# Kernel optimization log

Hardware: AMD Instinct MI355X
Metric: run time of the kernel (lower is better)

Reference implementation:

```python
import jax, jax.numpy as jnp
import numpy as np

B, I, O, S, C = 64, 2048, 2048, 10, 512  # batch, input, output, dendritic segments, context dim


def setup_inputs() -> dict:
    key = jax.random.key(0)
    ks = jax.random.split(key, 8)
    x = jax.random.normal(ks[0], (B, I), dtype=jnp.float32)
    context = jax.random.normal(ks[1], (B, C), dtype=jnp.float32)
    prev_activation = jax.random.normal(ks[2], (B, I), dtype=jnp.float32)
    # sparse-initialized weight: randn/sqrt(I) * (rand > sparsity)
    w = jax.random.normal(ks[3], (O, I), dtype=jnp.float32) / np.sqrt(I)
    mask = (jax.random.uniform(ks[4], (O, I)) > 0.9).astype(jnp.float32)
    weight = w * mask
    bias = jnp.zeros((O,), dtype=jnp.float32)
    astrocyte_activation = jnp.ones((O,), dtype=jnp.float32)
    astrocyte_threshold = jnp.full((O,), 0.5, dtype=jnp.float32)
    dendrite_segments = jax.random.normal(ks[5], (O, I, S), dtype=jnp.float32) / np.sqrt(I)
    dendritic_gates = jnp.ones((O, S), dtype=jnp.float32)
    connection_strength = jnp.ones((O, I), dtype=jnp.float32)
    pruning_threshold = jnp.full((1,), 0.01, dtype=jnp.float32)
    return {
        "x": x, "context": context, "prev_activation": prev_activation,
        "weight": weight, "bias": bias,
        "astrocyte_activation": astrocyte_activation,
        "astrocyte_threshold": astrocyte_threshold,
        "dendrite_segments": dendrite_segments,
        "dendritic_gates": dendritic_gates,
        "connection_strength": connection_strength,
        "pruning_threshold": pruning_threshold,
    }


def reference(x, context, prev_activation, weight, bias, astrocyte_activation,
              astrocyte_threshold, dendrite_segments, dendritic_gates,
              connection_strength, pruning_threshold):
    dt = x.dtype
    # structural plasticity (eval branch): prune weak connections
    conn_mask = (jnp.abs(weight) * connection_strength > pruning_threshold[0]).astype(dt)
    eff_w = weight * conn_mask  # [O, I]
    # astrocyte modulation
    ctx_signal = jnp.mean(context, axis=-1, keepdims=True)          # [B, 1]
    astro = jax.nn.sigmoid(ctx_signal * astrocyte_activation[None, :])  # [B, O]
    astro = astro * (astro > astrocyte_threshold[None, :]).astype(dt)
    mean_astro = jnp.mean(astro, axis=0)                            # [O]
    mod_w = eff_w * mean_astro[:, None]                             # [O, I]
    synaptic = x @ mod_w.T + bias                                   # [B, O]
    # multi-compartment dendritic processing
    seg_act = jnp.einsum('bi,ois->bos', x, dendrite_segments)       # [B, O, S]
    gated = jax.nn.relu(seg_act) * jax.nn.sigmoid(dendritic_gates)[None, :, :]
    dendritic = jnp.sum(gated, axis=-1)                             # [B, O]
    return jax.nn.relu(synaptic + dendritic)
```

## Files before the change

kernel.cpp:

```cpp
#include <hip/hip_runtime.h>
#include <math.h>

#define Bn 64
#define In 2048
#define On 2048
#define Sn 10
#define Cn 512

#define OT 4
#define KSPLIT 4
#define KRANGE (In / KSPLIT)
#define KT 64
#define NSTG (KRANGE / KT)
#define LROW 72
#define SLOT 12

typedef short short8 __attribute__((ext_vector_type(8)));
typedef float f32x4 __attribute__((ext_vector_type(4)));

__device__ __forceinline__ unsigned short f2bf(float f) {
    union { float f; unsigned u; } v; v.f = f;
    unsigned r = (v.u + 0x7FFFu + ((v.u >> 16) & 1u)) >> 16;
    return (unsigned short)r;
}

__global__ void prep_kernel(const float* __restrict__ x,
                            const float* __restrict__ ctx,
                            float* __restrict__ ws_ctx,
                            unsigned short* __restrict__ ws_xbf) {
    const int b = blockIdx.x;
    const int t = threadIdx.x;
    if (b < Bn) {
        __shared__ float red[256];
        red[t] = ctx[b * Cn + t] + ctx[b * Cn + t + 256];
        __syncthreads();
        for (int off = 128; off > 0; off >>= 1) {
            if (t < off) red[t] += red[t + off];
            __syncthreads();
        }
        if (t == 0) ws_ctx[b] = red[0] * (1.0f / (float)Cn);
    } else {
        int idx = (b - Bn) * 256 + t;
        ws_xbf[idx] = f2bf(x[idx]);
    }
}

__global__ void mastro_kernel(const float* __restrict__ aact,
                              const float* __restrict__ athr,
                              const float* __restrict__ ws_ctx,
                              float* __restrict__ ws_mastro) {
    const int o = blockIdx.x * 256 + threadIdx.x;
    const float aa = aact[o], th = athr[o];
    float sum = 0.0f;
    for (int b = 0; b < Bn; ++b) {
        float sg = 1.0f / (1.0f + expf(-ws_ctx[b] * aa));
        if (sg > th) sum += sg;
    }
    ws_mastro[o] = sum * (1.0f / (float)Bn);
}

__global__ __launch_bounds__(256, 8)
void main_kernel(const unsigned short* __restrict__ xbf,
                 const float* __restrict__ wgt,
                 const float* __restrict__ cst,
                 const float* __restrict__ seg,
                 const float* __restrict__ prn,
                 float* __restrict__ P) {
    __shared__ __align__(16) unsigned short Blds[2][48 * LROW];

    const int t = threadIdx.x;
    const int grp = blockIdx.x >> 2;
    const int ks  = blockIdx.x & 3;
    const int o0 = grp * OT;
    const int ib = ks * KRANGE;
    const int w = t >> 6, l = t & 63;
    const int l15 = l & 15, q = l >> 4;
    const float pthr = prn[0];

    for (int idx = t; idx < 4 * LROW; idx += 256) {
        Blds[0][44 * LROW + idx] = 0;
        Blds[1][44 * LROW + idx] = 0;
    }

    const int ii0 = (2 * l) / 10;
    const int s0  = (2 * l) % 10;

    float2 sv[5];
    float wv, cv;

    const float* segw = seg + (size_t)(o0 + w) * In * Sn;

    auto load_stage = [&](int is) {
        const float* sp = segw + (size_t)(ib + is * KT) * Sn + 2 * l;
#pragma unroll
        for (int c = 0; c < 5; ++c) sv[c] = *(const float2*)(sp + c * 128);
        wv = wgt[(size_t)(o0 + w) * In + ib + is * KT + l];
        cv = cst[(size_t)(o0 + w) * In + ib + is * KT + l];
    };

    auto store_stage = [&](int bb) {
        int ii = ii0, s = s0;
#pragma unroll
        for (int c = 0; c < 5; ++c) {
            unsigned short* bp = &Blds[bb][(w * Sn + s) * LROW + ii];
            bp[0]    = f2bf(sv[c].x);
            bp[LROW] = f2bf(sv[c].y);
            s += 8; ii += 12;
            if (s >= 10) { s -= 10; ++ii; }
        }
        float e = (__builtin_fabsf(wv) * cv > pthr) ? wv : 0.0f;
        Blds[bb][(40 + w) * LROW + l] = f2bf(e);
    };

    f32x4 acc[3];
#pragma unroll
    for (int n = 0; n < 3; ++n) acc[n] = (f32x4){0.f, 0.f, 0.f, 0.f};

    auto compute = [&](int bb, int is) {
        const unsigned short* xrow =
            xbf + (size_t)(w * 16 + l15) * In + ib + is * KT + q * 8;
#pragma unroll
        for (int kk = 0; kk < KT; kk += 32) {
            short8 a  = *(const short8*)(xrow + kk);
            short8 b0 = *(const short8*)&Blds[bb][(0  + l15) * LROW + q * 8 + kk];
            short8 b1 = *(const short8*)&Blds[bb][(16 + l15) * LROW + q * 8 + kk];
            short8 b2 = *(const short8*)&Blds[bb][(32 + l15) * LROW + q * 8 + kk];
            acc[0] = __builtin_amdgcn_mfma_f32_16x16x32_bf16(a, b0, acc[0], 0, 0, 0);
            acc[1] = __builtin_amdgcn_mfma_f32_16x16x32_bf16(a, b1, acc[1], 0, 0, 0);
            acc[2] = __builtin_amdgcn_mfma_f32_16x16x32_bf16(a, b2, acc[2], 0, 0, 0);
        }
    };

    load_stage(0);
    store_stage(0);
    load_stage(1);
    __syncthreads();
    for (int is = 0; is < NSTG; ++is) {
        compute(is & 1, is);
        if (is + 1 < NSTG) {
            store_stage((is + 1) & 1);
            if (is + 2 < NSTG) load_stage(is + 2);
        }
        __syncthreads();
    }

    float* scratch = (float*)&Blds[0][0] + w * (16 * 48);
#pragma unroll
    for (int nt = 0; nt < 3; ++nt) {
        const int n = nt * 16 + l15;
        if (n < 44) {
#pragma unroll
            for (int r = 0; r < 4; ++r)
                scratch[(q * 4 + r) * 48 + n] = acc[nt][r];
        }
    }
    __syncthreads();
    {
        const int mloc = l >> 2, ol = l & 3;
        const float* srow = (const float*)&Blds[0][0] + w * (16 * 48) + mloc * 48;
        float d[10];
#pragma unroll
        for (int s = 0; s < 10; ++s) d[s] = srow[ol * 10 + s];
        const float syn = srow[40 + ol];
        f32x4 p0 = {d[0], d[1], d[2], d[3]};
        f32x4 p1 = {d[4], d[5], d[6], d[7]};
        f32x4 p2 = {d[8], d[9], syn, 0.0f};
        const int m = w * 16 + mloc;
        float* pp = P + (((size_t)ks * Bn + m) * On + o0 + ol) * SLOT;
        *(f32x4*)(pp)     = p0;
        *(f32x4*)(pp + 4) = p1;
        *(f32x4*)(pp + 8) = p2;
    }
}

__global__ void finalize_kernel(const float* __restrict__ P,
                                const float* __restrict__ gates,
                                const float* __restrict__ bias,
                                const float* __restrict__ ws_mastro,
                                float* __restrict__ out) {
    const int t = threadIdx.x;
    const int o = (blockIdx.x & 31) * 64 + (t & 63);
    const int b = (blockIdx.x >> 5) * 4 + (t >> 6);
    f32x4 v0 = {0.f, 0.f, 0.f, 0.f}, v1 = v0, v2 = v0;
#pragma unroll
    for (int ks = 0; ks < KSPLIT; ++ks) {
        const f32x4* p = (const f32x4*)(P + (((size_t)ks * Bn + b) * On + o) * SLOT);
        v0 += p[0]; v1 += p[1]; v2 += p[2];
    }
    float d[12];
#pragma unroll
    for (int j = 0; j < 4; ++j) { d[j] = v0[j]; d[4 + j] = v1[j]; d[8 + j] = v2[j]; }
    float dend = 0.0f;
#pragma unroll
    for (int s = 0; s < Sn; ++s) {
        float g = 1.0f / (1.0f + expf(-gates[o * Sn + s]));
        float r = d[s] > 0.0f ? d[s] : 0.0f;
        dend += r * g;
    }
    float val = d[10] * ws_mastro[o] + bias[o] + dend;
    out[(size_t)b * On + o] = val > 0.0f ? val : 0.0f;
}

extern "C" void kernel_launch(void* const* d_in, const int* in_sizes, int n_in,
                              void* d_out, int out_size, void* d_ws, size_t ws_size,
                              hipStream_t stream) {
    (void)in_sizes; (void)n_in; (void)out_size; (void)ws_size;
    const float* x    = (const float*)d_in[0];
    const float* ctx  = (const float*)d_in[1];
    const float* wgt  = (const float*)d_in[3];
    const float* bias = (const float*)d_in[4];
    const float* aact = (const float*)d_in[5];
    const float* athr = (const float*)d_in[6];
    const float* seg  = (const float*)d_in[7];
    const float* gat  = (const float*)d_in[8];
    const float* cst  = (const float*)d_in[9];
    const float* prn  = (const float*)d_in[10];
    float* out = (float*)d_out;

    float* ws_ctx = (float*)d_ws;
    unsigned short* ws_xbf = (unsigned short*)((char*)d_ws + 256);
    float* ws_mastro = (float*)((char*)d_ws + 262400);
    float* ws_P = (float*)((char*)d_ws + 270592);

    prep_kernel<<<Bn + (Bn * In) / 256, 256, 0, stream>>>(x, ctx, ws_ctx, ws_xbf);
    mastro_kernel<<<On / 256, 256, 0, stream>>>(aact, athr, ws_ctx, ws_mastro);
    main_kernel<<<(On / OT) * KSPLIT, 256, 0, stream>>>(ws_xbf, wgt, cst, seg, prn, ws_P);
    finalize_kernel<<<(On / 64) * (Bn / 4), 256, 0, stream>>>(ws_P, gat, bias, ws_mastro, out);
}
```

Baseline: 301.2 us.

## Use single-wave blocks covering all batch tiles and drop barriers

Restructures main_kernel from four waves per block (one per output row and batch tile) to a single 64-thread wave. That wave loads segment, weight and connection data for all four outputs and runs all four 16-row batch MFMA tiles itself. Since one wave owns the LDS staging, the __syncthreads barriers are removed. The partial-sum buffer is reordered to [ks][o][b] and finalize is remapped so each block handles four outputs across all batches. The trade-off is more registers per thread and four times fewer threads in flight, which may hurt latency hiding on the memory-bound segment stream.

```diff
diff --git a/kernel.cpp b/kernel.cpp
--- a/kernel.cpp
+++ b/kernel.cpp
@@ -7,12 +7,12 @@
 #define Sn 10
 #define Cn 512
 
-#define OT 4
 #define KSPLIT 4
 #define KRANGE (In / KSPLIT)
 #define KT 64
 #define NSTG (KRANGE / KT)
 #define LROW 72
+#define SROW 50
 #define SLOT 12
 
 typedef short short8 __attribute__((ext_vector_type(8)));
@@ -59,7 +59,7 @@
     ws_mastro[o] = sum * (1.0f / (float)Bn);
 }
 
-__global__ __launch_bounds__(256, 8)
+__global__ __launch_bounds__(64, 2)
 void main_kernel(const unsigned short* __restrict__ xbf,
                  const float* __restrict__ wgt,
                  const float* __restrict__ cst,
@@ -68,16 +68,15 @@
                  float* __restrict__ P) {
     __shared__ __align__(16) unsigned short Blds[2][48 * LROW];
 
-    const int t = threadIdx.x;
+    const int l = threadIdx.x;
     const int grp = blockIdx.x >> 2;
     const int ks  = blockIdx.x & 3;
-    const int o0 = grp * OT;
+    const int o0 = grp * 4;
     const int ib = ks * KRANGE;
-    const int w = t >> 6, l = t & 63;
     const int l15 = l & 15, q = l >> 4;
     const float pthr = prn[0];
 
-    for (int idx = t; idx < 4 * LROW; idx += 256) {
+    for (int idx = l; idx < 4 * LROW; idx += 64) {
         Blds[0][44 * LROW + idx] = 0;
         Blds[1][44 * LROW + idx] = 0;
     }
@@ -85,79 +84,88 @@
     const int ii0 = (2 * l) / 10;
     const int s0  = (2 * l) % 10;
 
-    float2 sv[5];
-    float wv, cv;
-
-    const float* segw = seg + (size_t)(o0 + w) * In * Sn;
+    float2 sv[4][5];
+    float wv[4], cv[4];
 
     auto load_stage = [&](int is) {
-        const float* sp = segw + (size_t)(ib + is * KT) * Sn + 2 * l;
-#pragma unroll
-        for (int c = 0; c < 5; ++c) sv[c] = *(const float2*)(sp + c * 128);
-        wv = wgt[(size_t)(o0 + w) * In + ib + is * KT + l];
-        cv = cst[(size_t)(o0 + w) * In + ib + is * KT + l];
+        const int k0 = ib + is * KT;
+#pragma unroll
+        for (int oo = 0; oo < 4; ++oo) {
+            const float* sp = seg + ((size_t)(o0 + oo) * In + k0) * Sn + 2 * l;
+#pragma unroll
+            for (int c = 0; c < 5; ++c) sv[oo][c] = *(const float2*)(sp + c * 128);
+            wv[oo] = wgt[(size_t)(o0 + oo) * In + k0 + l];
+            cv[oo] = cst[(size_t)(o0 + oo) * In + k0 + l];
+        }
     };
 
     auto store_stage = [&](int bb) {
-        int ii = ii0, s = s0;
-#pragma unroll
-        for (int c = 0; c < 5; ++c) {
-            unsigned short* bp = &Blds[bb][(w * Sn + s) * LROW + ii];
-            bp[0]    = f2bf(sv[c].x);
-            bp[LROW] = f2bf(sv[c].y);
-            s += 8; ii += 12;
-            if (s >= 10) { s -= 10; ++ii; }
-        }
-        float e = (__builtin_fabsf(wv) * cv > pthr) ? wv : 0.0f;
-        Blds[bb][(40 + w) * LROW + l] = f2bf(e);
+#pragma unroll
+        for (int oo = 0; oo < 4; ++oo) {
+            int ii = ii0, s = s0;
+#pragma unroll
+            for (int c = 0; c < 5; ++c) {
+                unsigned short* bp = &Blds[bb][(oo * 10 + s) * LROW + ii];
+                bp[0]    = f2bf(sv[oo][c].x);
+                bp[LROW] = f2bf(sv[oo][c].y);
+                s += 8; ii += 12;
+                if (s >= 10) { s -= 10; ++ii; }
+            }
+            float e = (__builtin_fabsf(wv[oo]) * cv[oo] > pthr) ? wv[oo] : 0.0f;
+            Blds[bb][(40 + oo) * LROW + l] = f2bf(e);
+        }
     };
 
-    f32x4 acc[3];
-#pragma unroll
-    for (int n = 0; n < 3; ++n) acc[n] = (f32x4){0.f, 0.f, 0.f, 0.f};
+    f32x4 acc[12];
+#pragma unroll
+    for (int n = 0; n < 12; ++n) acc[n] = (f32x4){0.f, 0.f, 0.f, 0.f};
 
     auto compute = [&](int bb, int is) {
-        const unsigned short* xrow =
-            xbf + (size_t)(w * 16 + l15) * In + ib + is * KT + q * 8;
+        const int k0 = ib + is * KT;
 #pragma unroll
         for (int kk = 0; kk < KT; kk += 32) {
-            short8 a  = *(const short8*)(xrow + kk);
+            short8 a[4];
+#pragma unroll
+            for (int mt = 0; mt < 4; ++mt)
+                a[mt] = *(const short8*)(xbf + (size_t)(mt * 16 + l15) * In + k0 + q * 8 + kk);
             short8 b0 = *(const short8*)&Blds[bb][(0  + l15) * LROW + q * 8 + kk];
             short8 b1 = *(const short8*)&Blds[bb][(16 + l15) * LROW + q * 8 + kk];
             short8 b2 = *(const short8*)&Blds[bb][(32 + l15) * LROW + q * 8 + kk];
-            acc[0] = __builtin_amdgcn_mfma_f32_16x16x32_bf16(a, b0, acc[0], 0, 0, 0);
-            acc[1] = __builtin_amdgcn_mfma_f32_16x16x32_bf16(a, b1, acc[1], 0, 0, 0);
-            acc[2] = __builtin_amdgcn_mfma_f32_16x16x32_bf16(a, b2, acc[2], 0, 0, 0);
+#pragma unroll
+            for (int mt = 0; mt < 4; ++mt) {
+                acc[mt * 3 + 0] = __builtin_amdgcn_mfma_f32_16x16x32_bf16(a[mt], b0, acc[mt * 3 + 0], 0, 0, 0);
+                acc[mt * 3 + 1] = __builtin_amdgcn_mfma_f32_16x16x32_bf16(a[mt], b1, acc[mt * 3 + 1], 0, 0, 0);
+                acc[mt * 3 + 2] = __builtin_amdgcn_mfma_f32_16x16x32_bf16(a[mt], b2, acc[mt * 3 + 2], 0, 0, 0);
+            }
         }
     };
 
     load_stage(0);
     store_stage(0);
     load_stage(1);
-    __syncthreads();
     for (int is = 0; is < NSTG; ++is) {
         compute(is & 1, is);
         if (is + 1 < NSTG) {
             store_stage((is + 1) & 1);
             if (is + 2 < NSTG) load_stage(is + 2);
         }
-        __syncthreads();
-    }
-
-    float* scratch = (float*)&Blds[0][0] + w * (16 * 48);
-#pragma unroll
-    for (int nt = 0; nt < 3; ++nt) {
-        const int n = nt * 16 + l15;
-        if (n < 44) {
-#pragma unroll
-            for (int r = 0; r < 4; ++r)
-                scratch[(q * 4 + r) * 48 + n] = acc[nt][r];
-        }
-    }
-    __syncthreads();
-    {
-        const int mloc = l >> 2, ol = l & 3;
-        const float* srow = (const float*)&Blds[0][0] + w * (16 * 48) + mloc * 48;
+    }
+
+    float* scratch = (float*)&Blds[0][0];
+#pragma unroll
+    for (int mt = 0; mt < 4; ++mt)
+#pragma unroll
+        for (int nt = 0; nt < 3; ++nt) {
+            const int n = nt * 16 + l15;
+            if (n < 44) {
+#pragma unroll
+                for (int r = 0; r < 4; ++r)
+                    scratch[(mt * 16 + q * 4 + r) * SROW + n] = acc[mt * 3 + nt][r];
+            }
+        }
+    const float* srow = scratch + l * SROW;
+#pragma unroll
+    for (int ol = 0; ol < 4; ++ol) {
         float d[10];
 #pragma unroll
         for (int s = 0; s < 10; ++s) d[s] = srow[ol * 10 + s];
@@ -165,8 +173,7 @@
         f32x4 p0 = {d[0], d[1], d[2], d[3]};
         f32x4 p1 = {d[4], d[5], d[6], d[7]};
         f32x4 p2 = {d[8], d[9], syn, 0.0f};
-        const int m = w * 16 + mloc;
-        float* pp = P + (((size_t)ks * Bn + m) * On + o0 + ol) * SLOT;
+        float* pp = P + (((size_t)ks * On + o0 + ol) * Bn + l) * SLOT;
         *(f32x4*)(pp)     = p0;
         *(f32x4*)(pp + 4) = p1;
         *(f32x4*)(pp + 8) = p2;
@@ -179,12 +186,13 @@
                                 const float* __restrict__ ws_mastro,
                                 float* __restrict__ out) {
     const int t = threadIdx.x;
-    const int o = (blockIdx.x & 31) * 64 + (t & 63);
-    const int b = (blockIdx.x >> 5) * 4 + (t >> 6);
+    const int b = t & 63;
+    const int ol = t >> 6;
+    const int o = blockIdx.x * 4 + ol;
     f32x4 v0 = {0.f, 0.f, 0.f, 0.f}, v1 = v0, v2 = v0;
 #pragma unroll
     for (int ks = 0; ks < KSPLIT; ++ks) {
-        const f32x4* p = (const f32x4*)(P + (((size_t)ks * Bn + b) * On + o) * SLOT);
+        const f32x4* p = (const f32x4*)(P + (((size_t)ks * On + o) * Bn + b) * SLOT);
         v0 += p[0]; v1 += p[1]; v2 += p[2];
     }
     float d[12];
@@ -224,6 +232,6 @@
 
     prep_kernel<<<Bn + (Bn * In) / 256, 256, 0, stream>>>(x, ctx, ws_ctx, ws_xbf);
     mastro_kernel<<<On / 256, 256, 0, stream>>>(aact, athr, ws_ctx, ws_mastro);
-    main_kernel<<<(On / OT) * KSPLIT, 256, 0, stream>>>(ws_xbf, wgt, cst, seg, prn, ws_P);
-    finalize_kernel<<<(On / 64) * (Bn / 4), 256, 0, stream>>>(ws_P, gat, bias, ws_mastro, out);
-}
+    main_kernel<<<(On / 4) * KSPLIT, 64, 0, stream>>>(ws_xbf, wgt, cst, seg, prn, ws_P);
+    finalize_kernel<<<On / 4, 256, 0, stream>>>(ws_P, gat, bias, ws_mastro, out);
+}
```

After: 300.1 us. Within noise of the previous version (-0.4%).
